# Optimization experiments

Measured on AMD Instinct MI355X. Metric: run time of the kernel, lower is better.

Reference implementation:

```python
import jax, jax.numpy as jnp
import numpy as np

N = 100000   # nodes
E = 1600000  # edges
IN, H, OUT = 128, 128, 40
BN_EPS = 1e-5


def setup_inputs() -> dict:
    key = jax.random.key(0)
    ks = jax.random.split(key, 8)
    x = jax.random.normal(ks[0], (N, IN), jnp.float32)
    edge_src = jax.random.randint(ks[1], (E,), 0, N, jnp.int32)
    edge_dst = jax.random.randint(ks[2], (E,), 0, N, jnp.int32)

    def glorot(k, shape):
        lim = (6.0 / (shape[0] + shape[1])) ** 0.5
        return jax.random.uniform(k, shape, jnp.float32, -lim, lim)

    return {
        "x": x, "edge_src": edge_src, "edge_dst": edge_dst,
        "W1": glorot(ks[3], (IN, H)), "b1": jnp.zeros((H,), jnp.float32),
        "g1": jnp.ones((H,), jnp.float32), "bt1": jnp.zeros((H,), jnp.float32),
        "W2": glorot(ks[4], (H, H)), "b2": jnp.zeros((H,), jnp.float32),
        "g2": jnp.ones((H,), jnp.float32), "bt2": jnp.zeros((H,), jnp.float32),
        "Wr": glorot(ks[5], (H, OUT)), "br": jnp.zeros((OUT,), jnp.float32),
    }


def _gcn_conv(h_in, W, b, src, dst, dinv):
    # GCNConv: D^{-1/2}(A+I)D^{-1/2} X W + b  (symmetric norm w/ self-loops)
    h = h_in @ W                                   # [N,H]
    coef = dinv[src] * dinv[dst]                   # [E]
    agg = jax.ops.segment_sum(h[src] * coef[:, None], dst, num_segments=N)
    agg = agg + h * (dinv * dinv)[:, None]         # self-loop contribution
    return agg + b


def _bn_relu(h, gamma, beta):
    # BatchNorm1d in training mode (batch stats, biased variance) + ReLU
    mean = jnp.mean(h, axis=0)
    var = jnp.var(h, axis=0)
    y = (h - mean) * jax.lax.rsqrt(var + BN_EPS) * gamma + beta
    return jax.nn.relu(y)


def reference(x, edge_src, edge_dst, W1, b1, g1, bt1, W2, b2, g2, bt2, Wr, br):
    ones = jnp.ones((E,), jnp.float32)
    deg = jax.ops.segment_sum(ones, edge_dst, num_segments=N) + 1.0  # +1 self-loop
    dinv = jax.lax.rsqrt(deg)

    h = _gcn_conv(x, W1, b1, edge_src, edge_dst, dinv)
    h = _bn_relu(h, g1, bt1)
    h = _gcn_conv(h, W2, b2, edge_src, edge_dst, dinv)
    h = _bn_relu(h, g2, bt2)
    # dropout omitted (deterministic eval); readout linear
    return h @ Wr + br
```

## Files before the change

kernel.cpp:

```cpp
#include <hip/hip_runtime.h>
#include <hip/hip_bf16.h>
#include <hip/hip_fp16.h>

#define H_DIM 128

typedef _Float16 half8 __attribute__((ext_vector_type(8)));
typedef float floatx4 __attribute__((ext_vector_type(4)));

__global__ void degree_kernel(const int* __restrict__ dst, int* __restrict__ deg, int E_) {
    int i = blockIdx.x * blockDim.x + threadIdx.x;
    if (i < E_) atomicAdd(&deg[dst[i]], 1);
}

__global__ void scan_block_kernel(const int* __restrict__ deg, float* __restrict__ dinv,
                                  int* __restrict__ rowptr, int* __restrict__ bsum, int N_) {
    __shared__ int sh[256];
    int i = blockIdx.x * 256 + threadIdx.x;
    int v = (i < N_) ? deg[i] : 0;
    if (i < N_) dinv[i] = rsqrtf((float)v + 1.0f);
    sh[threadIdx.x] = v;
    __syncthreads();
    for (int off = 1; off < 256; off <<= 1) {
        int t = (threadIdx.x >= off) ? sh[threadIdx.x - off] : 0;
        __syncthreads();
        sh[threadIdx.x] += t;
        __syncthreads();
    }
    if (i < N_) rowptr[i] = sh[threadIdx.x] - v;
    if (threadIdx.x == 255) bsum[blockIdx.x] = sh[255];
}

__global__ void scan_bsums_kernel(const int* __restrict__ bsum, int* __restrict__ boff, int nb) {
    __shared__ int sh[512];
    int v = (threadIdx.x < nb) ? bsum[threadIdx.x] : 0;
    sh[threadIdx.x] = v;
    __syncthreads();
    for (int off = 1; off < 512; off <<= 1) {
        int t = (threadIdx.x >= off) ? sh[threadIdx.x - off] : 0;
        __syncthreads();
        sh[threadIdx.x] += t;
        __syncthreads();
    }
    if (threadIdx.x < nb) boff[threadIdx.x] = sh[threadIdx.x] - v;
}

__global__ void scan_add_kernel(int* __restrict__ rowptr, const int* __restrict__ boff,
                                int N_, int E_) {
    int i = blockIdx.x * 256 + threadIdx.x;
    if (i < N_) rowptr[i] += boff[blockIdx.x];
    if (i == 0) rowptr[N_] = E_;
}

__global__ void csr_fill_kernel(const int* __restrict__ src, const int* __restrict__ dst,
                                const int* __restrict__ rowptr, int* __restrict__ cursor,
                                int* __restrict__ cols, int E_, int N_, int shift) {
    int b = blockIdx.x & 7;
    if (((N_ - 1) >> shift) < b) return;
    int i = (blockIdx.x >> 3) * blockDim.x + threadIdx.x;
    if (i < E_) {
        int d = dst[i];
        if ((d >> shift) == b) {
            int p = rowptr[d] + atomicAdd(&cursor[d], 1);
            cols[p] = src[i];
        }
    }
}

__device__ inline half8 a_frag_f32(const float* Xr, int k0) {
    float4 v0 = *(const float4*)(Xr + k0);
    float4 v1 = *(const float4*)(Xr + k0 + 4);
    half8 a;
    a[0] = (_Float16)v0.x; a[1] = (_Float16)v0.y; a[2] = (_Float16)v0.z; a[3] = (_Float16)v0.w;
    a[4] = (_Float16)v1.x; a[5] = (_Float16)v1.y; a[6] = (_Float16)v1.z; a[7] = (_Float16)v1.w;
    return a;
}
__device__ inline half8 a_frag_f16_bn(const _Float16* Xr, int k0,
                                      const float* __restrict__ A, const float* __restrict__ B) {
    half8 r = *(const half8*)(Xr + k0);
    float4 a0 = *(const float4*)(A + k0);
    float4 a1 = *(const float4*)(A + k0 + 4);
    float4 b0 = *(const float4*)(B + k0);
    float4 b1 = *(const float4*)(B + k0 + 4);
    half8 o;
    o[0] = (_Float16)fmaxf(fmaf((float)r[0], a0.x, b0.x), 0.f);
    o[1] = (_Float16)fmaxf(fmaf((float)r[1], a0.y, b0.y), 0.f);
    o[2] = (_Float16)fmaxf(fmaf((float)r[2], a0.z, b0.z), 0.f);
    o[3] = (_Float16)fmaxf(fmaf((float)r[3], a0.w, b0.w), 0.f);
    o[4] = (_Float16)fmaxf(fmaf((float)r[4], a1.x, b1.x), 0.f);
    o[5] = (_Float16)fmaxf(fmaf((float)r[5], a1.y, b1.y), 0.f);
    o[6] = (_Float16)fmaxf(fmaf((float)r[6], a1.z, b1.z), 0.f);
    o[7] = (_Float16)fmaxf(fmaf((float)r[7], a1.w, b1.w), 0.f);
    return o;
}

template<bool BN, typename InT>
__global__ __launch_bounds__(256) void gemm_mfma_kernel(
    const InT* __restrict__ X, const float* __restrict__ W,
    const float* __restrict__ Abn, const float* __restrict__ Bbn,
    const float* __restrict__ dinv,
    _Float16* __restrict__ Y, int N_)
{
    __shared__ _Float16 Wf[32 * 64 * 8];

    const int tid = threadIdx.x;
    for (int idx = tid; idx < 128 * 32; idx += 256) {
        int k = idx >> 5;
        int n0 = (idx & 31) * 4;
        float4 w = *(const float4*)(W + k * 128 + n0);
        int kb = k >> 5, q = (k >> 3) & 3, j = k & 7;
#pragma unroll
        for (int u = 0; u < 4; ++u) {
            int n = n0 + u;
            int lane = (n & 15) | (q << 4);
            Wf[((((n >> 4) * 4 + kb) * 64 + lane) << 3) + j] = (_Float16)((&w.x)[u]);
        }
    }
    __syncthreads();

    const int wv = tid >> 6, lane = tid & 63;
    const int m = lane & 15, q = lane >> 4;
    const int row0 = blockIdx.x * 64 + wv * 16;

    int arow = row0 + m;
    if (arow >= N_) arow = N_ - 1;
    const InT* Xr = X + (size_t)arow * H_DIM;

    half8 a[4];
#pragma unroll
    for (int kb = 0; kb < 4; ++kb) {
        int k0 = kb * 32 + q * 8;
        if constexpr (BN) a[kb] = a_frag_f16_bn((const _Float16*)Xr, k0, Abn, Bbn);
        else              a[kb] = a_frag_f32((const float*)Xr, k0);
    }

    floatx4 acc[8];
#pragma unroll
    for (int nt = 0; nt < 8; ++nt) acc[nt] = (floatx4){0.f, 0.f, 0.f, 0.f};

#pragma unroll
    for (int nt = 0; nt < 8; ++nt) {
#pragma unroll
        for (int kb = 0; kb < 4; ++kb) {
            half8 b = *(const half8*)&Wf[(((nt * 4 + kb) * 64 + lane) << 3)];
            acc[nt] = __builtin_amdgcn_mfma_f32_16x16x32_f16(a[kb], b, acc[nt], 0, 0, 0);
        }
    }

#pragma unroll
    for (int r = 0; r < 4; ++r) {
        int row = row0 + q * 4 + r;
        if (row < N_) {
            float ds = dinv[row];
            _Float16* Yr = Y + (size_t)row * H_DIM + m;
#pragma unroll
            for (int nt = 0; nt < 8; ++nt)
                Yr[nt * 16] = (_Float16)(ds * acc[nt][r]);
        }
    }
}

__global__ __launch_bounds__(256) void readout_mfma_kernel(
    const _Float16* __restrict__ X, const float* __restrict__ W,
    const float* __restrict__ Abn, const float* __restrict__ Bbn,
    const float* __restrict__ br,
    float* __restrict__ Y, int N_, int OUTC)
{
    __shared__ _Float16 Wf[12 * 64 * 8];

    const int tid = threadIdx.x;
    for (int idx = tid; idx < 128 * 64; idx += 256) {
        int k = idx >> 6, n = idx & 63;
        if (n < 48) {
            float w = (n < OUTC) ? W[k * OUTC + n] : 0.f;
            int kb = k >> 5, q = (k >> 3) & 3, j = k & 7;
            int lane = (n & 15) | (q << 4);
            Wf[((((n >> 4) * 4 + kb) * 64 + lane) << 3) + j] = (_Float16)w;
        }
    }
    __syncthreads();

    const int wv = tid >> 6, lane = tid & 63;
    const int m = lane & 15, q = lane >> 4;
    const int row0 = blockIdx.x * 64 + wv * 16;

    int arow = row0 + m;
    if (arow >= N_) arow = N_ - 1;
    const _Float16* Xr = X + (size_t)arow * H_DIM;

    half8 a[4];
#pragma unroll
    for (int kb = 0; kb < 4; ++kb)
        a[kb] = a_frag_f16_bn(Xr, kb * 32 + q * 8, Abn, Bbn);

    floatx4 acc[3];
#pragma unroll
    for (int nt = 0; nt < 3; ++nt) acc[nt] = (floatx4){0.f, 0.f, 0.f, 0.f};

#pragma unroll
    for (int nt = 0; nt < 3; ++nt) {
#pragma unroll
        for (int kb = 0; kb < 4; ++kb) {
            half8 b = *(const half8*)&Wf[(((nt * 4 + kb) * 64 + lane) << 3)];
            acc[nt] = __builtin_amdgcn_mfma_f32_16x16x32_f16(a[kb], b, acc[nt], 0, 0, 0);
        }
    }

#pragma unroll
    for (int nt = 0; nt < 3; ++nt) {
        int col = nt * 16 + m;
        if (col < OUTC) {
            float bb = br[col];
#pragma unroll
            for (int r = 0; r < 4; ++r) {
                int row = row0 + q * 4 + r;
                if (row < N_)
                    Y[(size_t)row * OUTC + col] = acc[nt][r] + bb;
            }
        }
    }
}

__global__ __launch_bounds__(256) void aggregate_stats_kernel(
    const __half2* __restrict__ Gp,
    const int* __restrict__ rowptr,
    const int* __restrict__ cols,
    const float* __restrict__ dinv, const float* __restrict__ bias,
    __half2* __restrict__ out,
    float* __restrict__ gsum, float* __restrict__ gsq,
    int N_, int stride)
{
    const int wave = threadIdx.x >> 6;
    const int lane = threadIdx.x & 63;
    const int c = lane * 2;
    const float bs0 = bias[c], bs1 = bias[c + 1];
    const __half2 z = __float2half2_rn(0.f);

    float r0 = 0.f, r1 = 0.f, q0 = 0.f, q1 = 0.f;

    for (int n = blockIdx.x * 4 + wave; n < N_; n += stride) {
        __half2 acc[8];
        acc[0] = Gp[((unsigned)n << 6) | (unsigned)lane];
#pragma unroll
        for (int u = 1; u < 8; ++u) acc[u] = z;

        const int e0 = rowptr[n];
        const int e1 = rowptr[n + 1];
        for (int e = e0; e < e1; e += 16) {
            unsigned off[16];
#pragma unroll
            for (int u = 0; u < 16; ++u) {
                int ee = e + u;
                int id = cols[ee < e1 ? ee : e1 - 1];
                off[u] = ((unsigned)id << 6) | (unsigned)lane;
            }
            __half2 h[16];
#pragma unroll
            for (int u = 0; u < 16; ++u)
                h[u] = Gp[off[u]];
#pragma unroll
            for (int u = 0; u < 16; ++u)
                acc[u & 7] = __hadd2(acc[u & 7], (e + u < e1) ? h[u] : z);
        }

        __half2 p0 = __hadd2(__hadd2(acc[0], acc[1]), __hadd2(acc[2], acc[3]));
        __half2 p1 = __hadd2(__hadd2(acc[4], acc[5]), __hadd2(acc[6], acc[7]));
        float2 f0 = __half22float2(p0);
        float2 f1 = __half22float2(p1);
        float di = dinv[n];
        float o0 = fmaf(di, f0.x + f1.x, bs0);
        float o1 = fmaf(di, f0.y + f1.y, bs1);
        out[((unsigned)n << 6) | (unsigned)lane] = __floats2half2_rn(o0, o1);

        r0 += o0; r1 += o1;
        q0 = fmaf(o0, o0, q0); q1 = fmaf(o1, o1, q1);
    }

    __shared__ float ssum[4][128], ssq[4][128];
    ssum[wave][c] = r0; ssum[wave][c + 1] = r1;
    ssq[wave][c]  = q0; ssq[wave][c + 1]  = q1;
    __syncthreads();
    if (threadIdx.x < 128) {
        int k = threadIdx.x;
        float s = (ssum[0][k] + ssum[1][k]) + (ssum[2][k] + ssum[3][k]);
        float q = (ssq[0][k] + ssq[1][k]) + (ssq[2][k] + ssq[3][k]);
        atomicAdd(&gsum[k], s);
        atomicAdd(&gsq[k], q);
    }
}

__global__ __launch_bounds__(128) void bn_finalize_kernel(
    const float* __restrict__ sum, const float* __restrict__ sumsq,
    const float* __restrict__ gamma, const float* __restrict__ beta,
    float* __restrict__ A, float* __restrict__ B, int N_)
{
    int c = threadIdx.x;
    float inv_n = 1.0f / (float)N_;
    float mean = sum[c] * inv_n;
    float var = sumsq[c] * inv_n - mean * mean;
    float rstd = rsqrtf(var + 1e-5f);
    float a = rstd * gamma[c];
    A[c] = a;
    B[c] = beta[c] - mean * a;
}

extern "C" void kernel_launch(void* const* d_in, const int* in_sizes, int n_in,
                              void* d_out, int out_size, void* d_ws, size_t ws_size,
                              hipStream_t stream) {
    const float* x   = (const float*)d_in[0];
    const int* esrc  = (const int*)d_in[1];
    const int* edst  = (const int*)d_in[2];
    const float* W1  = (const float*)d_in[3];
    const float* b1  = (const float*)d_in[4];
    const float* g1  = (const float*)d_in[5];
    const float* bt1 = (const float*)d_in[6];
    const float* W2  = (const float*)d_in[7];
    const float* b2  = (const float*)d_in[8];
    const float* g2  = (const float*)d_in[9];
    const float* bt2 = (const float*)d_in[10];
    const float* Wr  = (const float*)d_in[11];
    const float* br  = (const float*)d_in[12];

    const int N_ = in_sizes[0] / H_DIM;
    const int E_ = in_sizes[1];
    const int OUTC = out_size / N_;

    char* p = (char*)d_ws;
    auto alloc = [&](size_t bytes) -> void* {
        void* r = (void*)p;
        p += (bytes + 255) & ~(size_t)255;
        return r;
    };
    __half* tmpA = (__half*)alloc((size_t)N_ * H_DIM * 2);
    __half* tmpB = (__half*)alloc((size_t)N_ * H_DIM * 2);
    int*   cols  = (int*)  alloc((size_t)E_ * 4);
    int*   rowptr= (int*)  alloc((size_t)(N_ + 1) * 4);
    size_t degcur_sz = ((size_t)2 * N_ * 4 + 255) & ~(size_t)255;
    int*   degcur= (int*)  alloc((size_t)2 * N_ * 4);
    float* bnbuf = (float*)alloc(8 * 128 * 4);
    int*   deg   = degcur;
    int*   cursor= degcur + N_;
    float* sum1 = bnbuf,       *sq1 = bnbuf + 128;
    float* sum2 = bnbuf + 256, *sq2 = bnbuf + 384;
    float* A1 = bnbuf + 512, *B1 = bnbuf + 640;
    float* A2 = bnbuf + 768, *B2 = bnbuf + 896;
    float* dinv  = (float*)alloc((size_t)N_ * 4);
    int*   bsum  = (int*)  alloc(4096);
    int*   boff  = (int*)  alloc(4096);

    hipMemsetAsync(degcur, 0, degcur_sz + 4 * 128 * 4, stream);

    const int nb = (N_ + 255) / 256;
    const int eb = (E_ + 255) / 256;
    const int ntiles64 = (N_ + 63) / 64;

    int shift = 0;
    while (((N_ - 1) >> shift) > 7) ++shift;

    const int AGG_BLOCKS = 2048;
    const int AGG_STRIDE = AGG_BLOCKS * 4;

    degree_kernel<<<eb, 256, 0, stream>>>(edst, deg, E_);
    scan_block_kernel<<<nb, 256, 0, stream>>>(deg, dinv, rowptr, bsum, N_);
    scan_bsums_kernel<<<1, 512, 0, stream>>>(bsum, boff, nb);
    scan_add_kernel<<<nb, 256, 0, stream>>>(rowptr, boff, N_, E_);
    csr_fill_kernel<<<eb * 8, 256, 0, stream>>>(esrc, edst, rowptr, cursor, cols, E_, N_, shift);

    gemm_mfma_kernel<false, float><<<ntiles64, 256, 0, stream>>>(
        x, W1, nullptr, nullptr, dinv, (_Float16*)tmpA, N_);
    aggregate_stats_kernel<<<AGG_BLOCKS, 256, 0, stream>>>(
        (const __half2*)tmpA, rowptr, cols, dinv, b1, (__half2*)tmpB,
        sum1, sq1, N_, AGG_STRIDE);
    bn_finalize_kernel<<<1, 128, 0, stream>>>(sum1, sq1, g1, bt1, A1, B1, N_);

    gemm_mfma_kernel<true, _Float16><<<ntiles64, 256, 0, stream>>>(
        (const _Float16*)tmpB, W2, A1, B1, dinv, (_Float16*)tmpA, N_);
    aggregate_stats_kernel<<<AGG_BLOCKS, 256, 0, stream>>>(
        (const __half2*)tmpA, rowptr, cols, dinv, b2, (__half2*)tmpB,
        sum2, sq2, N_, AGG_STRIDE);
    bn_finalize_kernel<<<1, 128, 0, stream>>>(sum2, sq2, g2, bt2, A2, B2, N_);

    readout_mfma_kernel<<<ntiles64, 256, 0, stream>>>(
        (const _Float16*)tmpB, Wr, A2, B2, br, (float*)d_out, N_, OUTC);
}
```

Before: 533.5 us.

## Software-pipeline CSR aggregation and fold BN finalize and scan into consumers

The aggregation kernel now prefetches the column indices and row pointers of upcoming nodes one and two iterations ahead. Each iteration gathers the first 24 neighbours in one batch, and a tail loop of 8 handles higher-degree nodes. The BatchNorm finalize kernels are removed and the coefficients are computed per block into LDS inside the GEMM and readout kernels. The separate block-sum scan kernel is replaced by a per-block reduction of earlier block sums. The intent is fewer kernel launches and more gather latency hidden, at the cost of higher register pressure and redundant per-block work.

```diff
diff --git a/kernel.cpp b/kernel.cpp
--- a/kernel.cpp
+++ b/kernel.cpp
@@ -30,24 +30,21 @@
     if (threadIdx.x == 255) bsum[blockIdx.x] = sh[255];
 }
 
-__global__ void scan_bsums_kernel(const int* __restrict__ bsum, int* __restrict__ boff, int nb) {
-    __shared__ int sh[512];
-    int v = (threadIdx.x < nb) ? bsum[threadIdx.x] : 0;
-    sh[threadIdx.x] = v;
+__global__ void scan_add_kernel(int* __restrict__ rowptr, const int* __restrict__ bsum,
+                                int N_, int E_) {
+    __shared__ int red[256];
+    const int b = blockIdx.x, t = threadIdx.x;
+    int s = 0;
+    for (int j = t; j < b; j += 256) s += bsum[j];
+    red[t] = s;
     __syncthreads();
-    for (int off = 1; off < 512; off <<= 1) {
-        int t = (threadIdx.x >= off) ? sh[threadIdx.x - off] : 0;
+    for (int off = 128; off > 0; off >>= 1) {
+        if (t < off) red[t] += red[t + off];
         __syncthreads();
-        sh[threadIdx.x] += t;
-        __syncthreads();
-    }
-    if (threadIdx.x < nb) boff[threadIdx.x] = sh[threadIdx.x] - v;
-}
-
-__global__ void scan_add_kernel(int* __restrict__ rowptr, const int* __restrict__ boff,
-                                int N_, int E_) {
-    int i = blockIdx.x * 256 + threadIdx.x;
-    if (i < N_) rowptr[i] += boff[blockIdx.x];
+    }
+    int boff = red[0];
+    int i = b * 256 + t;
+    if (i < N_) rowptr[i] += boff;
     if (i == 0) rowptr[N_] = E_;
 }
 
@@ -75,7 +72,7 @@
     return a;
 }
 __device__ inline half8 a_frag_f16_bn(const _Float16* Xr, int k0,
-                                      const float* __restrict__ A, const float* __restrict__ B) {
+                                      const float* A, const float* B) {
     half8 r = *(const half8*)(Xr + k0);
     float4 a0 = *(const float4*)(A + k0);
     float4 a1 = *(const float4*)(A + k0 + 4);
@@ -96,13 +93,25 @@
 template<bool BN, typename InT>
 __global__ __launch_bounds__(256) void gemm_mfma_kernel(
     const InT* __restrict__ X, const float* __restrict__ W,
-    const float* __restrict__ Abn, const float* __restrict__ Bbn,
+    const float* __restrict__ gsum, const float* __restrict__ gsq,
+    const float* __restrict__ gamma, const float* __restrict__ beta,
     const float* __restrict__ dinv,
     _Float16* __restrict__ Y, int N_)
 {
     __shared__ _Float16 Wf[32 * 64 * 8];
+    __shared__ __align__(16) float Alds[128], Blds[128];
 
     const int tid = threadIdx.x;
+    if constexpr (BN) {
+        if (tid < 128) {
+            float inv_n = 1.0f / (float)N_;
+            float mean = gsum[tid] * inv_n;
+            float var  = gsq[tid] * inv_n - mean * mean;
+            float a = rsqrtf(var + 1e-5f) * gamma[tid];
+            Alds[tid] = a;
+            Blds[tid] = beta[tid] - mean * a;
+        }
+    }
     for (int idx = tid; idx < 128 * 32; idx += 256) {
         int k = idx >> 5;
         int n0 = (idx & 31) * 4;
@@ -129,7 +138,7 @@
 #pragma unroll
     for (int kb = 0; kb < 4; ++kb) {
         int k0 = kb * 32 + q * 8;
-        if constexpr (BN) a[kb] = a_frag_f16_bn((const _Float16*)Xr, k0, Abn, Bbn);
+        if constexpr (BN) a[kb] = a_frag_f16_bn((const _Float16*)Xr, k0, Alds, Blds);
         else              a[kb] = a_frag_f32((const float*)Xr, k0);
     }
 
@@ -161,13 +170,23 @@
 
 __global__ __launch_bounds__(256) void readout_mfma_kernel(
     const _Float16* __restrict__ X, const float* __restrict__ W,
-    const float* __restrict__ Abn, const float* __restrict__ Bbn,
+    const float* __restrict__ gsum, const float* __restrict__ gsq,
+    const float* __restrict__ gamma, const float* __restrict__ beta,
     const float* __restrict__ br,
     float* __restrict__ Y, int N_, int OUTC)
 {
     __shared__ _Float16 Wf[12 * 64 * 8];
+    __shared__ __align__(16) float Alds[128], Blds[128];
 
     const int tid = threadIdx.x;
+    if (tid < 128) {
+        float inv_n = 1.0f / (float)N_;
+        float mean = gsum[tid] * inv_n;
+        float var  = gsq[tid] * inv_n - mean * mean;
+        float a = rsqrtf(var + 1e-5f) * gamma[tid];
+        Alds[tid] = a;
+        Blds[tid] = beta[tid] - mean * a;
+    }
     for (int idx = tid; idx < 128 * 64; idx += 256) {
         int k = idx >> 6, n = idx & 63;
         if (n < 48) {
@@ -190,7 +209,7 @@
     half8 a[4];
 #pragma unroll
     for (int kb = 0; kb < 4; ++kb)
-        a[kb] = a_frag_f16_bn(Xr, kb * 32 + q * 8, Abn, Bbn);
+        a[kb] = a_frag_f16_bn(Xr, kb * 32 + q * 8, Alds, Blds);
 
     floatx4 acc[3];
 #pragma unroll
@@ -231,53 +250,81 @@
 {
     const int wave = threadIdx.x >> 6;
     const int lane = threadIdx.x & 63;
-    const int c = lane * 2;
-    const float bs0 = bias[c], bs1 = bias[c + 1];
+    const int c2 = lane * 2;
+    const float bs0 = bias[c2], bs1 = bias[c2 + 1];
     const __half2 z = __float2half2_rn(0.f);
 
     float r0 = 0.f, r1 = 0.f, q0 = 0.f, q1 = 0.f;
 
-    for (int n = blockIdx.x * 4 + wave; n < N_; n += stride) {
+    const int n0 = blockIdx.x * 4 + wave;
+    int e0 = 0, e1 = 0, f0 = 0, f1 = 0;
+    int c[24];
+    if (n0 < N_) {
+        e0 = rowptr[n0]; e1 = rowptr[n0 + 1];
+        int n1 = n0 + stride; if (n1 > N_ - 1) n1 = N_ - 1;
+        f0 = rowptr[n1]; f1 = rowptr[n1 + 1];
+#pragma unroll
+        for (int u = 0; u < 24; ++u) {
+            int ee = e0 + u;
+            c[u] = (e1 > e0) ? cols[ee < e1 ? ee : e1 - 1] : 0;
+        }
+    }
+
+    for (int n = n0; n < N_; n += stride) {
+        __half2 self = Gp[((unsigned)n << 6) | (unsigned)lane];
+        __half2 h[24];
+#pragma unroll
+        for (int u = 0; u < 24; ++u)
+            h[u] = Gp[((unsigned)c[u] << 6) | (unsigned)lane];
+
+        int n2 = n + 2 * stride; if (n2 > N_ - 1) n2 = N_ - 1;
+        int g0 = rowptr[n2], g1 = rowptr[n2 + 1];
+
+        {
+            int ff0 = f0, ff1 = f1;
+#pragma unroll
+            for (int u = 0; u < 24; ++u) {
+                int ee = ff0 + u;
+                c[u] = (ff1 > ff0) ? cols[ee < ff1 ? ee : ff1 - 1] : 0;
+            }
+        }
+
         __half2 acc[8];
-        acc[0] = Gp[((unsigned)n << 6) | (unsigned)lane];
+        acc[0] = self;
 #pragma unroll
         for (int u = 1; u < 8; ++u) acc[u] = z;
-
-        const int e0 = rowptr[n];
-        const int e1 = rowptr[n + 1];
-        for (int e = e0; e < e1; e += 16) {
-            unsigned off[16];
-#pragma unroll
-            for (int u = 0; u < 16; ++u) {
-                int ee = e + u;
-                int id = cols[ee < e1 ? ee : e1 - 1];
-                off[u] = ((unsigned)id << 6) | (unsigned)lane;
-            }
-            __half2 h[16];
-#pragma unroll
-            for (int u = 0; u < 16; ++u)
-                h[u] = Gp[off[u]];
-#pragma unroll
-            for (int u = 0; u < 16; ++u)
-                acc[u & 7] = __hadd2(acc[u & 7], (e + u < e1) ? h[u] : z);
+#pragma unroll
+        for (int u = 0; u < 24; ++u)
+            acc[u & 7] = __hadd2(acc[u & 7], (e0 + u < e1) ? h[u] : z);
+
+        for (int e = e0 + 24; e < e1; e += 8) {
+            int cc[8];
+#pragma unroll
+            for (int u = 0; u < 8; ++u) { int ee = e + u; cc[u] = cols[ee < e1 ? ee : e1 - 1]; }
+#pragma unroll
+            for (int u = 0; u < 8; ++u) h[u] = Gp[((unsigned)cc[u] << 6) | (unsigned)lane];
+#pragma unroll
+            for (int u = 0; u < 8; ++u) acc[u] = __hadd2(acc[u], (e + u < e1) ? h[u] : z);
         }
 
         __half2 p0 = __hadd2(__hadd2(acc[0], acc[1]), __hadd2(acc[2], acc[3]));
         __half2 p1 = __hadd2(__hadd2(acc[4], acc[5]), __hadd2(acc[6], acc[7]));
-        float2 f0 = __half22float2(p0);
-        float2 f1 = __half22float2(p1);
+        float2 F0 = __half22float2(p0);
+        float2 F1 = __half22float2(p1);
         float di = dinv[n];
-        float o0 = fmaf(di, f0.x + f1.x, bs0);
-        float o1 = fmaf(di, f0.y + f1.y, bs1);
+        float o0 = fmaf(di, F0.x + F1.x, bs0);
+        float o1 = fmaf(di, F0.y + F1.y, bs1);
         out[((unsigned)n << 6) | (unsigned)lane] = __floats2half2_rn(o0, o1);
 
         r0 += o0; r1 += o1;
         q0 = fmaf(o0, o0, q0); q1 = fmaf(o1, o1, q1);
+
+        e0 = f0; e1 = f1; f0 = g0; f1 = g1;
     }
 
     __shared__ float ssum[4][128], ssq[4][128];
-    ssum[wave][c] = r0; ssum[wave][c + 1] = r1;
-    ssq[wave][c]  = q0; ssq[wave][c + 1]  = q1;
+    ssum[wave][c2] = r0; ssum[wave][c2 + 1] = r1;
+    ssq[wave][c2]  = q0; ssq[wave][c2 + 1]  = q1;
     __syncthreads();
     if (threadIdx.x < 128) {
         int k = threadIdx.x;
@@ -286,21 +333,6 @@
         atomicAdd(&gsum[k], s);
         atomicAdd(&gsq[k], q);
     }
-}
-
-__global__ __launch_bounds__(128) void bn_finalize_kernel(
-    const float* __restrict__ sum, const float* __restrict__ sumsq,
-    const float* __restrict__ gamma, const float* __restrict__ beta,
-    float* __restrict__ A, float* __restrict__ B, int N_)
-{
-    int c = threadIdx.x;
-    float inv_n = 1.0f / (float)N_;
-    float mean = sum[c] * inv_n;
-    float var = sumsq[c] * inv_n - mean * mean;
-    float rstd = rsqrtf(var + 1e-5f);
-    float a = rstd * gamma[c];
-    A[c] = a;
-    B[c] = beta[c] - mean * a;
 }
 
 extern "C" void kernel_launch(void* const* d_in, const int* in_sizes, int n_in,
@@ -341,11 +373,8 @@
     int*   cursor= degcur + N_;
     float* sum1 = bnbuf,       *sq1 = bnbuf + 128;
     float* sum2 = bnbuf + 256, *sq2 = bnbuf + 384;
-    float* A1 = bnbuf + 512, *B1 = bnbuf + 640;
-    float* A2 = bnbuf + 768, *B2 = bnbuf + 896;
     float* dinv  = (float*)alloc((size_t)N_ * 4);
     int*   bsum  = (int*)  alloc(4096);
-    int*   boff  = (int*)  alloc(4096);
 
     hipMemsetAsync(degcur, 0, degcur_sz + 4 * 128 * 4, stream);
 
@@ -361,24 +390,21 @@
 
     degree_kernel<<<eb, 256, 0, stream>>>(edst, deg, E_);
     scan_block_kernel<<<nb, 256, 0, stream>>>(deg, dinv, rowptr, bsum, N_);
-    scan_bsums_kernel<<<1, 512, 0, stream>>>(bsum, boff, nb);
-    scan_add_kernel<<<nb, 256, 0, stream>>>(rowptr, boff, N_, E_);
+    scan_add_kernel<<<nb, 256, 0, stream>>>(rowptr, bsum, N_, E_);
     csr_fill_kernel<<<eb * 8, 256, 0, stream>>>(esrc, edst, rowptr, cursor, cols, E_, N_, shift);
 
     gemm_mfma_kernel<false, float><<<ntiles64, 256, 0, stream>>>(
-        x, W1, nullptr, nullptr, dinv, (_Float16*)tmpA, N_);
+        x, W1, nullptr, nullptr, nullptr, nullptr, dinv, (_Float16*)tmpA, N_);
     aggregate_stats_kernel<<<AGG_BLOCKS, 256, 0, stream>>>(
         (const __half2*)tmpA, rowptr, cols, dinv, b1, (__half2*)tmpB,
         sum1, sq1, N_, AGG_STRIDE);
-    bn_finalize_kernel<<<1, 128, 0, stream>>>(sum1, sq1, g1, bt1, A1, B1, N_);
 
     gemm_mfma_kernel<true, _Float16><<<ntiles64, 256, 0, stream>>>(
-        (const _Float16*)tmpB, W2, A1, B1, dinv, (_Float16*)tmpA, N_);
+        (const _Float16*)tmpB, W2, sum1, sq1, g1, bt1, dinv, (_Float16*)tmpA, N_);
     aggregate_stats_kernel<<<AGG_BLOCKS, 256, 0, stream>>>(
         (const __half2*)tmpA, rowptr, cols, dinv, b2, (__half2*)tmpB,
         sum2, sq2, N_, AGG_STRIDE);
-    bn_finalize_kernel<<<1, 128, 0, stream>>>(sum2, sq2, g2, bt2, A2, B2, N_);
 
     readout_mfma_kernel<<<ntiles64, 256, 0, stream>>>(
-        (const _Float16*)tmpB, Wr, A2, B2, br, (float*)d_out, N_, OUTC);
-}
+        (const _Float16*)tmpB, Wr, sum2, sq2, g2, bt2, br, (float*)d_out, N_, OUTC);
+}
```

New measurement: 517.5 us. 1.03x faster.
